# Kernel optimization log

Measured on AMD Instinct MI355X. Metric: run time of the kernel, lower is better.

Reference implementation:

```python
import jax, jax.numpy as jnp
import numpy as np

B, S, D, H, FACTOR = 1, 2048, 1024, 16, 16
HD = D // H


def setup_inputs() -> dict:
    key = jax.random.key(0)
    ks = jax.random.split(key, 9)
    s = 1.0 / np.sqrt(D)
    u = lambda k, shape: jax.random.uniform(k, shape, jnp.float32, -s, s)
    return {
        "x": jax.random.normal(ks[0], (B, S, D), jnp.float32),
        "Wq": u(ks[1], (D, D)), "bq": u(ks[2], (D,)),
        "Wk": u(ks[3], (D, D)), "bk": u(ks[4], (D,)),
        "Wv": u(ks[5], (D, D)), "bv": u(ks[6], (D,)),
        "Wo": u(ks[7], (D, D)), "bo": u(ks[8], (D,)),
    }


def reference(x, Wq, bq, Wk, bk, Wv, bv, Wo, bo):
    b, s, d = x.shape
    h, hd = H, HD
    # projections -> [b, h, s, hd]
    q = (x @ Wq + bq).reshape(b, s, h, hd).transpose(0, 2, 1, 3)
    k = (x @ Wk + bk).reshape(b, s, h, hd).transpose(0, 2, 1, 3)
    v = (x @ Wv + bv).reshape(b, s, h, hd).transpose(0, 2, 1, 3)
    # dense scores [b, h, s, s]
    scores = jnp.einsum('bhqd,bhkd->bhqk', q, k) / np.sqrt(hd).astype(np.float32)
    # top-k along last dim, scatter into zeros (non-topk entries stay 0, as in torch code)
    vals, idx = jax.lax.top_k(scores, FACTOR)  # [b,h,s,FACTOR]
    flat_scores = scores.reshape(-1, s)
    rows = jnp.arange(flat_scores.shape[0])[:, None]
    sparse = jnp.zeros_like(flat_scores).at[rows, idx.reshape(-1, FACTOR)].set(
        vals.reshape(-1, FACTOR)).reshape(scores.shape)
    attn = jax.nn.softmax(sparse, axis=-1)  # softmax over sparse scores incl. zeros
    out = jnp.einsum('bhqk,bhkd->bhqd', attn, v)
    out = out.transpose(0, 2, 1, 3).reshape(b, s, d)
    return out @ Wo + bo
```

## Files before the change

### kernel.cpp

```cpp
#include <hip/hip_runtime.h>
#include <stdint.h>

constexpr int SEQ  = 2048;
constexpr int DIM  = 1024;
constexpr int NH   = 16;
constexpr int HDIM = 64;
constexpr int TOPK = 16;
constexpr int CAP  = 128;
constexpr int CST  = 129;

typedef unsigned short bf16_t;
typedef __attribute__((ext_vector_type(8))) short bf16x8;
typedef __attribute__((ext_vector_type(4))) float f32x4;
typedef unsigned long long u64;

__device__ __forceinline__ int swzc(int col, int row) { return col ^ ((row & 7) << 3); }

__device__ __forceinline__ float bf2f(bf16_t b) {
  return __uint_as_float(((unsigned)b) << 16);
}
__device__ __forceinline__ bf16_t f2bf(float f) {
  unsigned u = __float_as_uint(f);
  unsigned r = u + 0x7fffu + ((u >> 16) & 1u);
  return (bf16_t)(r >> 16);
}
__device__ __forceinline__ f32x4 zero4() {
  f32x4 z; z[0] = 0.f; z[1] = 0.f; z[2] = 0.f; z[3] = 0.f; return z;
}
__device__ __forceinline__ void gload_lds16(const bf16_t* g, bf16_t* l) {
  __builtin_amdgcn_global_load_lds(
      (const __attribute__((address_space(1))) void*)g,
      (__attribute__((address_space(3))) void*)l, 16, 0, 0);
}
__device__ __forceinline__ unsigned ordf(float f) {
  unsigned b = __float_as_uint(f);
  return (b & 0x80000000u) ? ~b : (b | 0x80000000u);
}
__device__ __forceinline__ float iordf(unsigned u) {
  unsigned b = (u & 0x80000000u) ? (u ^ 0x80000000u) : ~u;
  return __uint_as_float(b);
}

__global__ void prep_kernel(const float* __restrict__ x, bf16_t* __restrict__ xb,
                            const float* __restrict__ W0, const float* __restrict__ W1,
                            const float* __restrict__ W2, const float* __restrict__ W3,
                            bf16_t* __restrict__ T0, bf16_t* __restrict__ T1,
                            bf16_t* __restrict__ T2, bf16_t* __restrict__ T3) {
  const int z = blockIdx.z;
  if (z == 4) {
    int bl = blockIdx.y * 32 + blockIdx.x;
    int tt = threadIdx.y * 32 + threadIdx.x;
    int i = (bl * 256 + tt) * 8;
    float4 v0 = *reinterpret_cast<const float4*>(x + i);
    float4 v1 = *reinterpret_cast<const float4*>(x + i + 4);
    bf16x8 o;
    o[0] = (short)f2bf(v0.x); o[1] = (short)f2bf(v0.y);
    o[2] = (short)f2bf(v0.z); o[3] = (short)f2bf(v0.w);
    o[4] = (short)f2bf(v1.x); o[5] = (short)f2bf(v1.y);
    o[6] = (short)f2bf(v1.z); o[7] = (short)f2bf(v1.w);
    *reinterpret_cast<bf16x8*>(xb + i) = o;
    return;
  }
  const float* W = (z == 0) ? W0 : (z == 1) ? W1 : (z == 2) ? W2 : W3;
  bf16_t* WT = (z == 0) ? T0 : (z == 1) ? T1 : (z == 2) ? T2 : T3;
  __shared__ float tile[32][33];
  int tx = threadIdx.x, ty = threadIdx.y;
  int bx = blockIdx.x * 32, by = blockIdx.y * 32;
#pragma unroll
  for (int i = 0; i < 4; ++i)
    tile[ty + i * 8][tx] = W[(by + ty + i * 8) * DIM + bx + tx];
  __syncthreads();
#pragma unroll
  for (int i = 0; i < 4; ++i)
    WT[(bx + ty + i * 8) * DIM + by + tx] = f2bf(tile[tx][ty + i * 8]);
}

template <int OUT_F32, int DO_SUMV>
__global__ __launch_bounds__(256) void gemm128(const bf16_t* __restrict__ A,
                                               const bf16_t* __restrict__ B0,
                                               const bf16_t* __restrict__ B1,
                                               const bf16_t* __restrict__ B2,
                                               const float* __restrict__ c0,
                                               const float* __restrict__ c1,
                                               const float* __restrict__ c2,
                                               void* __restrict__ o0,
                                               void* __restrict__ o1,
                                               void* __restrict__ o2,
                                               float* __restrict__ sumv) {
  __shared__ __align__(16) bf16_t As[2][128 * 64];
  __shared__ __align__(16) bf16_t Bs[2][64 * 64];
  const int t = threadIdx.x;
  const int which = blockIdx.x >> 4;
  const bf16_t* Bt = (which == 0) ? B0 : (which == 1) ? B1 : B2;
  const float* bias = (which == 0) ? c0 : (which == 1) ? c1 : c2;
  void* out = (which == 0) ? o0 : (which == 1) ? o1 : o2;
  const int bm0 = blockIdx.y * 128, bn0 = (blockIdx.x & 15) * 64;
  const int w = t >> 6, lane = t & 63, lr = lane & 15, lg = lane >> 4;
  const int wm = w >> 1, wn = w & 1;
  const int srow = t >> 3;
  const int scol = swzc((t & 7) * 8, srow);
  const int ldst = srow * 64 + (t & 7) * 8;
  const int rsw = (lr & 7) << 3;

  f32x4 acc[4][2];
#pragma unroll
  for (int m = 0; m < 4; ++m)
#pragma unroll
    for (int n = 0; n < 2; ++n) acc[m][n] = zero4();

#pragma unroll
  for (int i = 0; i < 4; ++i)
    gload_lds16(A + (bm0 + i * 32 + srow) * DIM + scol, &As[0][i * 32 * 64 + ldst]);
#pragma unroll
  for (int i = 0; i < 2; ++i)
    gload_lds16(Bt + (bn0 + i * 32 + srow) * DIM + scol, &Bs[0][i * 32 * 64 + ldst]);
  __syncthreads();

  for (int kt = 0; kt < 16; ++kt) {
    const int cur = kt & 1;
    if (kt < 15) {
#pragma unroll
      for (int i = 0; i < 4; ++i)
        gload_lds16(A + (bm0 + i * 32 + srow) * DIM + (kt + 1) * 64 + scol,
                    &As[cur ^ 1][i * 32 * 64 + ldst]);
#pragma unroll
      for (int i = 0; i < 2; ++i)
        gload_lds16(Bt + (bn0 + i * 32 + srow) * DIM + (kt + 1) * 64 + scol,
                    &Bs[cur ^ 1][i * 32 * 64 + ldst]);
    }
    bf16x8 a[4][2], b[2][2];
#pragma unroll
    for (int m = 0; m < 4; ++m)
#pragma unroll
      for (int kk = 0; kk < 2; ++kk)
        a[m][kk] = *reinterpret_cast<const bf16x8*>(
            &As[cur][(wm * 64 + m * 16 + lr) * 64 + ((kk * 32 + lg * 8) ^ rsw)]);
#pragma unroll
    for (int n = 0; n < 2; ++n)
#pragma unroll
      for (int kk = 0; kk < 2; ++kk)
        b[n][kk] = *reinterpret_cast<const bf16x8*>(
            &Bs[cur][(wn * 32 + n * 16 + lr) * 64 + ((kk * 32 + lg * 8) ^ rsw)]);
#pragma unroll
    for (int m = 0; m < 4; ++m)
#pragma unroll
      for (int n = 0; n < 2; ++n)
#pragma unroll
        for (int kk = 0; kk < 2; ++kk)
          acc[m][n] = __builtin_amdgcn_mfma_f32_16x16x32_bf16(a[m][kk], b[n][kk],
                                                              acc[m][n], 0, 0, 0);
    __syncthreads();
  }

#pragma unroll
  for (int n = 0; n < 2; ++n) {
    int col = bn0 + wn * 32 + n * 16 + lr;
    float bv = bias[col];
    float colsum = 0.f;
#pragma unroll
    for (int m = 0; m < 4; ++m)
#pragma unroll
      for (int r = 0; r < 4; ++r) {
        int row = bm0 + wm * 64 + m * 16 + lg * 4 + r;
        float val = acc[m][n][r] + bv;
        if (OUT_F32) {
          reinterpret_cast<float*>(out)[(size_t)row * DIM + col] = val;
        } else {
          bf16_t rb = f2bf(val);
          reinterpret_cast<bf16_t*>(out)[(size_t)row * DIM + col] = rb;
          if (DO_SUMV) colsum += bf2f(rb);
        }
      }
    if (DO_SUMV && which == 2) atomicAdd(&sumv[col], colsum);
  }
}

#define LOADK(buf, kc)                                                              \
  do {                                                                              \
    _Pragma("unroll") for (int n_ = 0; n_ < 4; ++n_)                                \
      _Pragma("unroll") for (int k_ = 0; k_ < 2; ++k_)                              \
        kf[buf][n_][k_] = *reinterpret_cast<const bf16x8*>(                         \
            kp + (size_t)((kc) * 64 + n_ * 16 + lr) * DIM + k_ * 32 + lg * 8);      \
  } while (0)

__global__ __launch_bounds__(256, 2) void attn_kernel(const bf16_t* __restrict__ q,
                                                      const bf16_t* __restrict__ k,
                                                      const bf16_t* __restrict__ v,
                                                      const float* __restrict__ sumv,
                                                      bf16_t* __restrict__ op) {
  __shared__ float CM[64 * 33];
  __shared__ float Tsh[64];
  __shared__ float zsh[64];
  __shared__ int   cnt[64];
  __shared__ u64   ckey[64 * CST];

  const int t = threadIdx.x;
  const int lin = blockIdx.x;
  const int xcd = lin & 7, ixd = lin >> 3;
  const int h = xcd * 2 + (ixd >> 5), qt = ixd & 31;
  const int w = t >> 6, lane = t & 63, lr = lane & 15, lg = lane >> 4;

  const bf16_t* qp = q + (size_t)(qt * 64) * DIM + h * HDIM;
  const bf16_t* kp = k + h * HDIM;

  bf16x8 aq[4][2];
#pragma unroll
  for (int m = 0; m < 4; ++m)
#pragma unroll
    for (int kk = 0; kk < 2; ++kk)
      aq[m][kk] = *reinterpret_cast<const bf16x8*>(
          qp + (size_t)(m * 16 + lr) * DIM + kk * 32 + lg * 8);

  bf16x8 kf[2][4][2];

  LOADK(0, w * 8);
#pragma unroll
  for (int i = 0; i < 8; ++i) {
    if (i < 7) LOADK((i + 1) & 1, w * 8 + i + 1);
    const int cur = i & 1;
    f32x4 sacc[4][4];
#pragma unroll
    for (int m = 0; m < 4; ++m)
#pragma unroll
      for (int n = 0; n < 4; ++n) sacc[m][n] = zero4();
#pragma unroll
    for (int m = 0; m < 4; ++m)
#pragma unroll
      for (int n = 0; n < 4; ++n)
#pragma unroll
        for (int kk = 0; kk < 2; ++kk)
          sacc[m][n] = __builtin_amdgcn_mfma_f32_16x16x32_bf16(aq[m][kk], kf[cur][n][kk],
                                                               sacc[m][n], 0, 0, 0);
    float mx[4][4];
#pragma unroll
    for (int m = 0; m < 4; ++m)
#pragma unroll
      for (int r = 0; r < 4; ++r)
        mx[m][r] = fmaxf(fmaxf(sacc[m][0][r], sacc[m][1][r]),
                         fmaxf(sacc[m][2][r], sacc[m][3][r]));
#pragma unroll
    for (int off = 1; off < 16; off <<= 1)
#pragma unroll
      for (int m = 0; m < 4; ++m)
#pragma unroll
        for (int r = 0; r < 4; ++r)
          mx[m][r] = fmaxf(mx[m][r], __shfl_xor(mx[m][r], off));
    if (lr == 0) {
#pragma unroll
      for (int m = 0; m < 4; ++m)
#pragma unroll
        for (int r = 0; r < 4; ++r)
          CM[(m * 16 + lg * 4 + r) * 33 + (w * 8 + i)] = mx[m][r] * 0.125f;
    }
  }
  LOADK(0, w * 8);
  __syncthreads();

  {
    const int trow = t >> 2, tsub = t & 3;
    float cmv[8];
#pragma unroll
    for (int c = 0; c < 8; ++c) cmv[c] = CM[trow * 33 + tsub * 8 + c];
    float Tval = -1e30f;
#pragma unroll
    for (int it = 0; it < TOPK; ++it) {
      float lm = cmv[0];
#pragma unroll
      for (int c = 1; c < 8; ++c) lm = fmaxf(lm, cmv[c]);
      float gm = fmaxf(lm, __shfl_xor(lm, 1));
      gm = fmaxf(gm, __shfl_xor(gm, 2));
      u64 b = __ballot(lm == gm);
      int base = lane & ~3;
      int ownsub = __ffsll((b >> base) & 0xFull) - 1;
      if (tsub == ownsub) {
        bool d = false;
#pragma unroll
        for (int c = 0; c < 8; ++c)
          if (!d && cmv[c] == lm) { cmv[c] = -1e30f; d = true; }
      }
      Tval = gm;
    }
    if (tsub == 0) { Tsh[trow] = Tval; cnt[trow] = 0; }
  }
  __syncthreads();

  float Treg[4][4];
#pragma unroll
  for (int m = 0; m < 4; ++m)
#pragma unroll
    for (int r = 0; r < 4; ++r) Treg[m][r] = Tsh[m * 16 + lg * 4 + r];

#pragma unroll
  for (int i = 0; i < 8; ++i) {
    if (i < 7) LOADK((i + 1) & 1, w * 8 + i + 1);
    const int cur = i & 1;
    const int kc = w * 8 + i;
    f32x4 sacc[4][4];
#pragma unroll
    for (int m = 0; m < 4; ++m)
#pragma unroll
      for (int n = 0; n < 4; ++n) sacc[m][n] = zero4();
#pragma unroll
    for (int m = 0; m < 4; ++m)
#pragma unroll
      for (int n = 0; n < 4; ++n)
#pragma unroll
        for (int kk = 0; kk < 2; ++kk)
          sacc[m][n] = __builtin_amdgcn_mfma_f32_16x16x32_bf16(aq[m][kk], kf[cur][n][kk],
                                                               sacc[m][n], 0, 0, 0);
#pragma unroll
    for (int m = 0; m < 4; ++m)
#pragma unroll
      for (int n = 0; n < 4; ++n)
#pragma unroll
        for (int r = 0; r < 4; ++r) {
          float val = sacc[m][n][r] * 0.125f;
          if (val >= Treg[m][r]) {
            int row = m * 16 + lg * 4 + r;
            int p = atomicAdd(&cnt[row], 1);
            if (p < CAP) {
              unsigned idx = (unsigned)(kc * 64 + n * 16 + lr);
              ckey[row * CST + p] = ((u64)ordf(val) << 32) | (u64)(~idx);
            }
          }
        }
  }
  __syncthreads();

  {
    const int trow = t >> 2, tsub = t & 3;
    int nc = cnt[trow]; if (nc > CAP) nc = CAP;
    float Zexp = 0.f;
    for (int sel = 0; sel < TOPK; ++sel) {
      u64 lmax = 0ull; int lp = -1;
      for (int p = tsub; p < nc; p += 4) {
        u64 kk2 = ckey[trow * CST + p];
        if (kk2 > lmax) { lmax = kk2; lp = p; }
      }
      u64 o1 = __shfl_xor(lmax, 1);
      u64 g1 = (o1 > lmax) ? o1 : lmax;
      u64 o2 = __shfl_xor(g1, 2);
      u64 gkey = (o2 > g1) ? o2 : g1;
      if (lmax == gkey && lp >= 0) ckey[trow * CST + lp] = 0ull;
      float val = iordf((unsigned)(gkey >> 32));
      int idx = (int)(~(unsigned)(gkey & 0xffffffffull));
      float e = expf(val);
      Zexp += e;
      if (tsub == 0) {
        CM[trow * 33 + sel] = e - 1.f;
        CM[trow * 33 + 16 + sel] = __int_as_float(idx);
      }
    }
    if (tsub == 0) zsh[trow] = 2032.f + Zexp;
  }
  __syncthreads();

  {
    const int row = t >> 2;
    const int dbase = h * HDIM + (t & 3) * 16;
    float oacc[16];
    const float4* sp = reinterpret_cast<const float4*>(sumv + dbase);
#pragma unroll
    for (int u = 0; u < 4; ++u) {
      float4 s4 = sp[u];
      oacc[u * 4 + 0] = s4.x; oacc[u * 4 + 1] = s4.y;
      oacc[u * 4 + 2] = s4.z; oacc[u * 4 + 3] = s4.w;
    }
    float invZ = 1.f / zsh[row];
#pragma unroll
    for (int j = 0; j < TOPK; ++j) {
      float wj = CM[row * 33 + j];
      int kidx = __float_as_int(CM[row * 33 + 16 + j]);
      const bf16x8* vp = reinterpret_cast<const bf16x8*>(v + (size_t)kidx * DIM + dbase);
      bf16x8 v0 = vp[0], v1 = vp[1];
#pragma unroll
      for (int e = 0; e < 8; ++e) {
        oacc[e] += wj * bf2f((bf16_t)v0[e]);
        oacc[8 + e] += wj * bf2f((bf16_t)v1[e]);
      }
    }
    bf16x8 o0, o1;
#pragma unroll
    for (int e = 0; e < 8; ++e) {
      o0[e] = (short)f2bf(oacc[e] * invZ);
      o1[e] = (short)f2bf(oacc[8 + e] * invZ);
    }
    bf16_t* orow = op + (size_t)(qt * 64 + row) * DIM + dbase;
    *reinterpret_cast<bf16x8*>(orow) = o0;
    *reinterpret_cast<bf16x8*>(orow + 8) = o1;
  }
}

extern "C" void kernel_launch(void* const* d_in, const int* in_sizes, int n_in,
                              void* d_out, int out_size, void* d_ws, size_t ws_size,
                              hipStream_t stream) {
  const float* x  = (const float*)d_in[0];
  const float* Wq = (const float*)d_in[1];
  const float* bq = (const float*)d_in[2];
  const float* Wk = (const float*)d_in[3];
  const float* bk = (const float*)d_in[4];
  const float* Wv = (const float*)d_in[5];
  const float* bv = (const float*)d_in[6];
  const float* Wo = (const float*)d_in[7];
  const float* bo = (const float*)d_in[8];
  float* out = (float*)d_out;

  char* ws = (char*)d_ws;
  bf16_t* xb   = (bf16_t*)(ws + (size_t)(0)  * (1 << 20));
  bf16_t* WqT  = (bf16_t*)(ws + (size_t)(4)  * (1 << 20));
  bf16_t* WkT  = (bf16_t*)(ws + (size_t)(6)  * (1 << 20));
  bf16_t* WvT  = (bf16_t*)(ws + (size_t)(8)  * (1 << 20));
  bf16_t* WoT  = (bf16_t*)(ws + (size_t)(10) * (1 << 20));
  bf16_t* qb   = (bf16_t*)(ws + (size_t)(12) * (1 << 20));
  bf16_t* kb   = (bf16_t*)(ws + (size_t)(16) * (1 << 20));
  bf16_t* vb   = (bf16_t*)(ws + (size_t)(20) * (1 << 20));
  bf16_t* opb  = (bf16_t*)(ws + (size_t)(24) * (1 << 20));
  float*  sumv = (float*) (ws + (size_t)(28) * (1 << 20));

  prep_kernel<<<dim3(32, 32, 5), dim3(32, 8), 0, stream>>>(x, xb, Wq, Wk, Wv, Wo,
                                                           WqT, WkT, WvT, WoT);
  hipMemsetAsync(sumv, 0, DIM * sizeof(float), stream);

  gemm128<0, 1><<<dim3(48, 16), 256, 0, stream>>>(xb, WqT, WkT, WvT, bq, bk, bv,
                                                  (void*)qb, (void*)kb, (void*)vb, sumv);

  attn_kernel<<<512, 256, 0, stream>>>(qb, kb, vb, sumv, opb);

  gemm128<1, 0><<<dim3(16, 16), 256, 0, stream>>>(opb, WoT, WoT, WoT, bo, bo, bo,
                                                  (void*)out, (void*)out, (void*)out, sumv);
}
```

Before: 206.6 us.

## Use 128x128 GEMM tiles, split-K output GEMM, and 32-row attention blocks

The QKV GEMM now uses 128x128 tiles, which gives more MFMA work per staged load and halves the grid. The output projection uses 128x128 tiles with a two-way split-K that accumulates into a zeroed output through float atomics, which adds a memset and atomic traffic. The attention kernel now handles 32 query rows per block, swaps the MFMA operand order so the per-row max reduction is simpler, stores candidates as separate float and short arrays with a smaller capacity, and raises occupancy to 4 blocks per CU. The smaller candidate capacity risks overflow if more than 96 scores pass the threshold.

Result: slower. 255.3 us (+23.6%).

```diff
diff --git a/kernel.cpp b/kernel.cpp
--- a/kernel.cpp
+++ b/kernel.cpp
@@ -6,8 +6,9 @@
 constexpr int NH   = 16;
 constexpr int HDIM = 64;
 constexpr int TOPK = 16;
-constexpr int CAP  = 128;
-constexpr int CST  = 129;
+constexpr int CAP  = 96;
+constexpr int CST  = 97;
+constexpr int QR   = 32;
 
 typedef unsigned short bf16_t;
 typedef __attribute__((ext_vector_type(8))) short bf16x8;
@@ -75,26 +76,31 @@
     WT[(bx + ty + i * 8) * DIM + by + tx] = f2bf(tile[tx][ty + i * 8]);
 }
 
-template <int OUT_F32, int DO_SUMV>
-__global__ __launch_bounds__(256) void gemm128(const bf16_t* __restrict__ A,
-                                               const bf16_t* __restrict__ B0,
-                                               const bf16_t* __restrict__ B1,
-                                               const bf16_t* __restrict__ B2,
-                                               const float* __restrict__ c0,
-                                               const float* __restrict__ c1,
-                                               const float* __restrict__ c2,
-                                               void* __restrict__ o0,
-                                               void* __restrict__ o1,
-                                               void* __restrict__ o2,
-                                               float* __restrict__ sumv) {
+template <int MODE>
+__global__ __launch_bounds__(256) void gemm_t(const bf16_t* __restrict__ A,
+                                              const bf16_t* __restrict__ B0,
+                                              const bf16_t* __restrict__ B1,
+                                              const bf16_t* __restrict__ B2,
+                                              const float* __restrict__ c0,
+                                              const float* __restrict__ c1,
+                                              const float* __restrict__ c2,
+                                              void* __restrict__ o0,
+                                              void* __restrict__ o1,
+                                              void* __restrict__ o2,
+                                              float* __restrict__ sumv) {
   __shared__ __align__(16) bf16_t As[2][128 * 64];
-  __shared__ __align__(16) bf16_t Bs[2][64 * 64];
+  __shared__ __align__(16) bf16_t Bs[2][128 * 64];
   const int t = threadIdx.x;
-  const int which = blockIdx.x >> 4;
+  int which, bn0, ks0, nst;
+  if (MODE == 0) {
+    which = blockIdx.x >> 3; bn0 = (blockIdx.x & 7) * 128; ks0 = 0; nst = 16;
+  } else {
+    which = 0; bn0 = blockIdx.x * 128; ks0 = blockIdx.z * 8; nst = 8;
+  }
   const bf16_t* Bt = (which == 0) ? B0 : (which == 1) ? B1 : B2;
   const float* bias = (which == 0) ? c0 : (which == 1) ? c1 : c2;
   void* out = (which == 0) ? o0 : (which == 1) ? o1 : o2;
-  const int bm0 = blockIdx.y * 128, bn0 = (blockIdx.x & 15) * 64;
+  const int bm0 = blockIdx.y * 128;
   const int w = t >> 6, lane = t & 63, lr = lane & 15, lg = lane >> 4;
   const int wm = w >> 1, wn = w & 1;
   const int srow = t >> 3;
@@ -102,33 +108,29 @@
   const int ldst = srow * 64 + (t & 7) * 8;
   const int rsw = (lr & 7) << 3;
 
-  f32x4 acc[4][2];
+  f32x4 acc[4][4];
 #pragma unroll
   for (int m = 0; m < 4; ++m)
 #pragma unroll
-    for (int n = 0; n < 2; ++n) acc[m][n] = zero4();
-
-#pragma unroll
-  for (int i = 0; i < 4; ++i)
-    gload_lds16(A + (bm0 + i * 32 + srow) * DIM + scol, &As[0][i * 32 * 64 + ldst]);
-#pragma unroll
-  for (int i = 0; i < 2; ++i)
-    gload_lds16(Bt + (bn0 + i * 32 + srow) * DIM + scol, &Bs[0][i * 32 * 64 + ldst]);
-  __syncthreads();
-
-  for (int kt = 0; kt < 16; ++kt) {
-    const int cur = kt & 1;
-    if (kt < 15) {
-#pragma unroll
-      for (int i = 0; i < 4; ++i)
-        gload_lds16(A + (bm0 + i * 32 + srow) * DIM + (kt + 1) * 64 + scol,
-                    &As[cur ^ 1][i * 32 * 64 + ldst]);
-#pragma unroll
-      for (int i = 0; i < 2; ++i)
-        gload_lds16(Bt + (bn0 + i * 32 + srow) * DIM + (kt + 1) * 64 + scol,
-                    &Bs[cur ^ 1][i * 32 * 64 + ldst]);
-    }
-    bf16x8 a[4][2], b[2][2];
+    for (int n = 0; n < 4; ++n) acc[m][n] = zero4();
+
+#define STAGE_G(buf, kt)                                                             \
+  do {                                                                               \
+    _Pragma("unroll") for (int i_ = 0; i_ < 4; ++i_) {                               \
+      gload_lds16(A + (size_t)(bm0 + i_ * 32 + srow) * DIM + (kt) * 64 + scol,       \
+                  &As[buf][i_ * 32 * 64 + ldst]);                                    \
+      gload_lds16(Bt + (size_t)(bn0 + i_ * 32 + srow) * DIM + (kt) * 64 + scol,      \
+                  &Bs[buf][i_ * 32 * 64 + ldst]);                                    \
+    }                                                                                \
+  } while (0)
+
+  STAGE_G(0, ks0);
+  __syncthreads();
+
+  for (int s = 0; s < nst; ++s) {
+    const int cur = s & 1;
+    if (s < nst - 1) STAGE_G(cur ^ 1, ks0 + s + 1);
+    bf16x8 a[4][2], b[4][2];
 #pragma unroll
     for (int m = 0; m < 4; ++m)
 #pragma unroll
@@ -136,42 +138,50 @@
         a[m][kk] = *reinterpret_cast<const bf16x8*>(
             &As[cur][(wm * 64 + m * 16 + lr) * 64 + ((kk * 32 + lg * 8) ^ rsw)]);
 #pragma unroll
-    for (int n = 0; n < 2; ++n)
+    for (int n = 0; n < 4; ++n)
 #pragma unroll
       for (int kk = 0; kk < 2; ++kk)
         b[n][kk] = *reinterpret_cast<const bf16x8*>(
-            &Bs[cur][(wn * 32 + n * 16 + lr) * 64 + ((kk * 32 + lg * 8) ^ rsw)]);
+            &Bs[cur][(wn * 64 + n * 16 + lr) * 64 + ((kk * 32 + lg * 8) ^ rsw)]);
 #pragma unroll
     for (int m = 0; m < 4; ++m)
 #pragma unroll
-      for (int n = 0; n < 2; ++n)
+      for (int n = 0; n < 4; ++n)
 #pragma unroll
         for (int kk = 0; kk < 2; ++kk)
           acc[m][n] = __builtin_amdgcn_mfma_f32_16x16x32_bf16(a[m][kk], b[n][kk],
                                                               acc[m][n], 0, 0, 0);
     __syncthreads();
   }
-
-#pragma unroll
-  for (int n = 0; n < 2; ++n) {
-    int col = bn0 + wn * 32 + n * 16 + lr;
+#undef STAGE_G
+
+#pragma unroll
+  for (int n = 0; n < 4; ++n) {
+    int col = bn0 + wn * 64 + n * 16 + lr;
     float bv = bias[col];
-    float colsum = 0.f;
-#pragma unroll
-    for (int m = 0; m < 4; ++m)
-#pragma unroll
-      for (int r = 0; r < 4; ++r) {
-        int row = bm0 + wm * 64 + m * 16 + lg * 4 + r;
-        float val = acc[m][n][r] + bv;
-        if (OUT_F32) {
-          reinterpret_cast<float*>(out)[(size_t)row * DIM + col] = val;
-        } else {
-          bf16_t rb = f2bf(val);
+    if (MODE == 0) {
+      float colsum = 0.f;
+#pragma unroll
+      for (int m = 0; m < 4; ++m)
+#pragma unroll
+        for (int r = 0; r < 4; ++r) {
+          int row = bm0 + wm * 64 + m * 16 + lg * 4 + r;
+          bf16_t rb = f2bf(acc[m][n][r] + bv);
           reinterpret_cast<bf16_t*>(out)[(size_t)row * DIM + col] = rb;
-          if (DO_SUMV) colsum += bf2f(rb);
+          if (which == 2) colsum += bf2f(rb);
         }
-      }
-    if (DO_SUMV && which == 2) atomicAdd(&sumv[col], colsum);
+      if (which == 2) atomicAdd(&sumv[col], colsum);
+    } else {
+      float badd = (ks0 == 0) ? bv : 0.f;
+#pragma unroll
+      for (int m = 0; m < 4; ++m)
+#pragma unroll
+        for (int r = 0; r < 4; ++r) {
+          int row = bm0 + wm * 64 + m * 16 + lg * 4 + r;
+          atomicAdd(reinterpret_cast<float*>(out) + (size_t)row * DIM + col,
+                    acc[m][n][r] + badd);
+        }
+    }
   }
 }
 
@@ -183,29 +193,30 @@
             kp + (size_t)((kc) * 64 + n_ * 16 + lr) * DIM + k_ * 32 + lg * 8);      \
   } while (0)
 
-__global__ __launch_bounds__(256, 2) void attn_kernel(const bf16_t* __restrict__ q,
+__global__ __launch_bounds__(256, 4) void attn_kernel(const bf16_t* __restrict__ q,
                                                       const bf16_t* __restrict__ k,
                                                       const bf16_t* __restrict__ v,
                                                       const float* __restrict__ sumv,
                                                       bf16_t* __restrict__ op) {
-  __shared__ float CM[64 * 33];
-  __shared__ float Tsh[64];
-  __shared__ float zsh[64];
-  __shared__ int   cnt[64];
-  __shared__ u64   ckey[64 * CST];
+  __shared__ float CM[QR * 33];
+  __shared__ float Tsh[QR];
+  __shared__ float zsh[QR];
+  __shared__ int   cnt[QR];
+  __shared__ float cval[QR * CST];
+  __shared__ unsigned short cidx[QR * CST];
 
   const int t = threadIdx.x;
   const int lin = blockIdx.x;
   const int xcd = lin & 7, ixd = lin >> 3;
-  const int h = xcd * 2 + (ixd >> 5), qt = ixd & 31;
+  const int h = xcd * 2 + (ixd >> 6), qt = ixd & 63;
   const int w = t >> 6, lane = t & 63, lr = lane & 15, lg = lane >> 4;
 
-  const bf16_t* qp = q + (size_t)(qt * 64) * DIM + h * HDIM;
+  const bf16_t* qp = q + (size_t)(qt * QR) * DIM + h * HDIM;
   const bf16_t* kp = k + h * HDIM;
 
-  bf16x8 aq[4][2];
-#pragma unroll
-  for (int m = 0; m < 4; ++m)
+  bf16x8 aq[2][2];
+#pragma unroll
+  for (int m = 0; m < 2; ++m)
 #pragma unroll
     for (int kk = 0; kk < 2; ++kk)
       aq[m][kk] = *reinterpret_cast<const bf16x8*>(
@@ -218,64 +229,53 @@
   for (int i = 0; i < 8; ++i) {
     if (i < 7) LOADK((i + 1) & 1, w * 8 + i + 1);
     const int cur = i & 1;
-    f32x4 sacc[4][4];
-#pragma unroll
-    for (int m = 0; m < 4; ++m)
+    f32x4 sacc[2][4];
+#pragma unroll
+    for (int m = 0; m < 2; ++m)
 #pragma unroll
       for (int n = 0; n < 4; ++n) sacc[m][n] = zero4();
 #pragma unroll
-    for (int m = 0; m < 4; ++m)
+    for (int m = 0; m < 2; ++m)
 #pragma unroll
       for (int n = 0; n < 4; ++n)
 #pragma unroll
         for (int kk = 0; kk < 2; ++kk)
-          sacc[m][n] = __builtin_amdgcn_mfma_f32_16x16x32_bf16(aq[m][kk], kf[cur][n][kk],
+          sacc[m][n] = __builtin_amdgcn_mfma_f32_16x16x32_bf16(kf[cur][n][kk], aq[m][kk],
                                                                sacc[m][n], 0, 0, 0);
-    float mx[4][4];
-#pragma unroll
-    for (int m = 0; m < 4; ++m)
-#pragma unroll
-      for (int r = 0; r < 4; ++r)
-        mx[m][r] = fmaxf(fmaxf(sacc[m][0][r], sacc[m][1][r]),
-                         fmaxf(sacc[m][2][r], sacc[m][3][r]));
-#pragma unroll
-    for (int off = 1; off < 16; off <<= 1)
-#pragma unroll
-      for (int m = 0; m < 4; ++m)
-#pragma unroll
-        for (int r = 0; r < 4; ++r)
-          mx[m][r] = fmaxf(mx[m][r], __shfl_xor(mx[m][r], off));
-    if (lr == 0) {
-#pragma unroll
-      for (int m = 0; m < 4; ++m)
-#pragma unroll
-        for (int r = 0; r < 4; ++r)
-          CM[(m * 16 + lg * 4 + r) * 33 + (w * 8 + i)] = mx[m][r] * 0.125f;
+#pragma unroll
+    for (int m = 0; m < 2; ++m) {
+      float mx = sacc[m][0][0];
+#pragma unroll
+      for (int n = 0; n < 4; ++n)
+#pragma unroll
+        for (int r = 0; r < 4; ++r) mx = fmaxf(mx, sacc[m][n][r]);
+      mx = fmaxf(mx, __shfl_xor(mx, 16));
+      mx = fmaxf(mx, __shfl_xor(mx, 32));
+      if (lane < 16) CM[(m * 16 + lane) * 33 + (w * 8 + i)] = mx * 0.125f;
     }
   }
   LOADK(0, w * 8);
   __syncthreads();
 
   {
-    const int trow = t >> 2, tsub = t & 3;
-    float cmv[8];
-#pragma unroll
-    for (int c = 0; c < 8; ++c) cmv[c] = CM[trow * 33 + tsub * 8 + c];
+    const int trow = t >> 3, tsub = t & 7;
+    float cmv[4];
+#pragma unroll
+    for (int c = 0; c < 4; ++c) cmv[c] = CM[trow * 33 + tsub * 4 + c];
     float Tval = -1e30f;
 #pragma unroll
     for (int it = 0; it < TOPK; ++it) {
-      float lm = cmv[0];
-#pragma unroll
-      for (int c = 1; c < 8; ++c) lm = fmaxf(lm, cmv[c]);
+      float lm = fmaxf(fmaxf(cmv[0], cmv[1]), fmaxf(cmv[2], cmv[3]));
       float gm = fmaxf(lm, __shfl_xor(lm, 1));
       gm = fmaxf(gm, __shfl_xor(gm, 2));
+      gm = fmaxf(gm, __shfl_xor(gm, 4));
       u64 b = __ballot(lm == gm);
-      int base = lane & ~3;
-      int ownsub = __ffsll((b >> base) & 0xFull) - 1;
+      int base = lane & ~7;
+      int ownsub = __ffsll((b >> base) & 0xFFull) - 1;
       if (tsub == ownsub) {
         bool d = false;
 #pragma unroll
-        for (int c = 0; c < 8; ++c)
+        for (int c = 0; c < 4; ++c)
           if (!d && cmv[c] == lm) { cmv[c] = -1e30f; d = true; }
       }
       Tval = gm;
@@ -284,43 +284,41 @@
   }
   __syncthreads();
 
-  float Treg[4][4];
-#pragma unroll
-  for (int m = 0; m < 4; ++m)
-#pragma unroll
-    for (int r = 0; r < 4; ++r) Treg[m][r] = Tsh[m * 16 + lg * 4 + r];
+  float Treg[2];
+#pragma unroll
+  for (int m = 0; m < 2; ++m) Treg[m] = Tsh[m * 16 + lr];
 
 #pragma unroll
   for (int i = 0; i < 8; ++i) {
     if (i < 7) LOADK((i + 1) & 1, w * 8 + i + 1);
     const int cur = i & 1;
     const int kc = w * 8 + i;
-    f32x4 sacc[4][4];
-#pragma unroll
-    for (int m = 0; m < 4; ++m)
+    f32x4 sacc[2][4];
+#pragma unroll
+    for (int m = 0; m < 2; ++m)
 #pragma unroll
       for (int n = 0; n < 4; ++n) sacc[m][n] = zero4();
 #pragma unroll
-    for (int m = 0; m < 4; ++m)
+    for (int m = 0; m < 2; ++m)
 #pragma unroll
       for (int n = 0; n < 4; ++n)
 #pragma unroll
         for (int kk = 0; kk < 2; ++kk)
-          sacc[m][n] = __builtin_amdgcn_mfma_f32_16x16x32_bf16(aq[m][kk], kf[cur][n][kk],
+          sacc[m][n] = __builtin_amdgcn_mfma_f32_16x16x32_bf16(kf[cur][n][kk], aq[m][kk],
                                                                sacc[m][n], 0, 0, 0);
 #pragma unroll
-    for (int m = 0; m < 4; ++m)
+    for (int m = 0; m < 2; ++m)
 #pragma unroll
       for (int n = 0; n < 4; ++n)
 #pragma unroll
         for (int r = 0; r < 4; ++r) {
           float val = sacc[m][n][r] * 0.125f;
-          if (val >= Treg[m][r]) {
-            int row = m * 16 + lg * 4 + r;
+          if (val >= Treg[m]) {
+            int row = m * 16 + lr;
             int p = atomicAdd(&cnt[row], 1);
             if (p < CAP) {
-              unsigned idx = (unsigned)(kc * 64 + n * 16 + lr);
-              ckey[row * CST + p] = ((u64)ordf(val) << 32) | (u64)(~idx);
+              cval[row * CST + p] = val;
+              cidx[row * CST + p] = (unsigned short)(kc * 64 + n * 16 + lg * 4 + r);
             }
           }
         }
@@ -328,22 +326,26 @@
   __syncthreads();
 
   {
-    const int trow = t >> 2, tsub = t & 3;
+    const int trow = t >> 3, tsub = t & 7;
     int nc = cnt[trow]; if (nc > CAP) nc = CAP;
     float Zexp = 0.f;
     for (int sel = 0; sel < TOPK; ++sel) {
       u64 lmax = 0ull; int lp = -1;
-      for (int p = tsub; p < nc; p += 4) {
-        u64 kk2 = ckey[trow * CST + p];
-        if (kk2 > lmax) { lmax = kk2; lp = p; }
+      for (int p = tsub; p < nc; p += 8) {
+        float vv = cval[trow * CST + p];
+        unsigned id = cidx[trow * CST + p];
+        u64 key = ((u64)ordf(vv) << 32) | (u64)(unsigned)(~id);
+        if (key > lmax) { lmax = key; lp = p; }
       }
-      u64 o1 = __shfl_xor(lmax, 1);
-      u64 g1 = (o1 > lmax) ? o1 : lmax;
-      u64 o2 = __shfl_xor(g1, 2);
-      u64 gkey = (o2 > g1) ? o2 : g1;
-      if (lmax == gkey && lp >= 0) ckey[trow * CST + lp] = 0ull;
-      float val = iordf((unsigned)(gkey >> 32));
-      int idx = (int)(~(unsigned)(gkey & 0xffffffffull));
+      u64 g = lmax;
+#pragma unroll
+      for (int d = 1; d < 8; d <<= 1) {
+        u64 o = __shfl_xor(g, d);
+        g = (o > g) ? o : g;
+      }
+      if (lmax == g && lp >= 0) cval[trow * CST + lp] = -1e30f;
+      float val = iordf((unsigned)(g >> 32));
+      int idx = (int)(~(unsigned)(g & 0xffffffffull));
       float e = expf(val);
       Zexp += e;
       if (tsub == 0) {
@@ -356,38 +358,26 @@
   __syncthreads();
 
   {
-    const int row = t >> 2;
-    const int dbase = h * HDIM + (t & 3) * 16;
-    float oacc[16];
+    const int row = t >> 3;
+    const int dbase = h * HDIM + (t & 7) * 8;
+    float oacc[8];
     const float4* sp = reinterpret_cast<const float4*>(sumv + dbase);
-#pragma unroll
-    for (int u = 0; u < 4; ++u) {
-      float4 s4 = sp[u];
-      oacc[u * 4 + 0] = s4.x; oacc[u * 4 + 1] = s4.y;
-      oacc[u * 4 + 2] = s4.z; oacc[u * 4 + 3] = s4.w;
-    }
+    float4 s0 = sp[0], s1 = sp[1];
+    oacc[0] = s0.x; oacc[1] = s0.y; oacc[2] = s0.z; oacc[3] = s0.w;
+    oacc[4] = s1.x; oacc[5] = s1.y; oacc[6] = s1.z; oacc[7] = s1.w;
     float invZ = 1.f / zsh[row];
 #pragma unroll
     for (int j = 0; j < TOPK; ++j) {
       float wj = CM[row * 33 + j];
       int kidx = __float_as_int(CM[row * 33 + 16 + j]);
-      const bf16x8* vp = reinterpret_cast<const bf16x8*>(v + (size_t)kidx * DIM + dbase);
-      bf16x8 v0 = vp[0], v1 = vp[1];
-#pragma unroll
-      for (int e = 0; e < 8; ++e) {
-        oacc[e] += wj * bf2f((bf16_t)v0[e]);
-        oacc[8 + e] += wj * bf2f((bf16_t)v1[e]);
-      }
+      bf16x8 vv = *reinterpret_cast<const bf16x8*>(v + (size_t)kidx * DIM + dbase);
+#pragma unroll
+      for (int e = 0; e < 8; ++e) oacc[e] += wj * bf2f((bf16_t)vv[e]);
     }
-    bf16x8 o0, o1;
-#pragma unroll
-    for (int e = 0; e < 8; ++e) {
-      o0[e] = (short)f2bf(oacc[e] * invZ);
-      o1[e] = (short)f2bf(oacc[8 + e] * invZ);
-    }
-    bf16_t* orow = op + (size_t)(qt * 64 + row) * DIM + dbase;
-    *reinterpret_cast<bf16x8*>(orow) = o0;
-    *reinterpret_cast<bf16x8*>(orow + 8) = o1;
+    bf16x8 o0;
+#pragma unroll
+    for (int e = 0; e < 8; ++e) o0[e] = (short)f2bf(oacc[e] * invZ);
+    *reinterpret_cast<bf16x8*>(op + (size_t)(qt * QR + row) * DIM + dbase) = o0;
   }
 }
 
@@ -420,12 +410,13 @@
   prep_kernel<<<dim3(32, 32, 5), dim3(32, 8), 0, stream>>>(x, xb, Wq, Wk, Wv, Wo,
                                                            WqT, WkT, WvT, WoT);
   hipMemsetAsync(sumv, 0, DIM * sizeof(float), stream);
-
-  gemm128<0, 1><<<dim3(48, 16), 256, 0, stream>>>(xb, WqT, WkT, WvT, bq, bk, bv,
-                                                  (void*)qb, (void*)kb, (void*)vb, sumv);
-
-  attn_kernel<<<512, 256, 0, stream>>>(qb, kb, vb, sumv, opb);
-
-  gemm128<1, 0><<<dim3(16, 16), 256, 0, stream>>>(opb, WoT, WoT, WoT, bo, bo, bo,
-                                                  (void*)out, (void*)out, (void*)out, sumv);
-}
+  hipMemsetAsync(out, 0, (size_t)SEQ * DIM * sizeof(float), stream);
+
+  gemm_t<0><<<dim3(24, 16), 256, 0, stream>>>(xb, WqT, WkT, WvT, bq, bk, bv,
+                                              (void*)qb, (void*)kb, (void*)vb, sumv);
+
+  attn_kernel<<<1024, 256, 0, stream>>>(qb, kb, vb, sumv, opb);
+
+  gemm_t<1><<<dim3(8, 16, 2), 256, 0, stream>>>(opb, WoT, WoT, WoT, bo, bo, bo,
+                                                (void*)out, (void*)out, (void*)out, sumv);
+}
```
